# Kernel optimization log

Measured on AMD Instinct MI355X. Metric: run time of the kernel, lower is better.

Reference implementation:

```python
import jax, jax.numpy as jnp
import numpy as np

NUM_FIELDS = 26

def setup_inputs() -> dict:
    key = jax.random.key(0)
    ks = jax.random.split(key, 8)
    B, F, D, V, d, af = 4096, NUM_FIELDS, 13, 100000, 64, 64
    return {
        "sparse_feat": jax.random.randint(ks[0], (B, F), 0, V, dtype=jnp.int32),
        "dense_feat": jax.random.uniform(ks[1], (B, D), dtype=jnp.float32),
        "embed_table": jax.random.normal(ks[2], (V, d), dtype=jnp.float32) * 0.05,
        "lin_table": jax.random.normal(ks[3], (V,), dtype=jnp.float32) * 0.05,
        "w_dense": jax.random.normal(ks[4], (D,), dtype=jnp.float32) * 0.1,
        "bias": jnp.zeros((1,), dtype=jnp.float32),
        "W1": jax.random.normal(ks[5], (d, af), dtype=jnp.float32) * (1.0 / np.sqrt(d)),
        "b1": jnp.zeros((af,), dtype=jnp.float32),
        "w2": jax.random.normal(ks[6], (af,), dtype=jnp.float32) * (1.0 / np.sqrt(af)),
        "p": jax.random.normal(ks[7], (d,), dtype=jnp.float32) * (1.0 / np.sqrt(d)),
    }

def reference(sparse_feat, dense_feat, embed_table, lin_table, w_dense, bias, W1, b1, w2, p):
    # Embedding lookup: [B, F, d]
    emb = embed_table[sparse_feat]
    # Linear part: per-field scalar weights + dense linear + bias -> [B]
    linear_out = lin_table[sparse_feat].sum(axis=1) + dense_feat @ w_dense + bias[0]
    # Pairwise interactions i<j (static indices): [B, P, d]
    i_idx, j_idx = np.triu_indices(NUM_FIELDS, k=1)
    att_x = emb[:, i_idx, :] * emb[:, j_idx, :]
    # Attention MLP: Linear(d, af) + ReLU + Linear(af, 1, no bias) -> [B, P]
    h = jax.nn.relu(jnp.einsum('bpd,da->bpa', att_x, W1) + b1)
    att_w = jnp.einsum('bpa,a->bp', h, w2)
    att_score = jax.nn.softmax(att_w, axis=1)
    # Softmax-weighted sum over pairs -> [B, d], then final projection p -> [B]
    att_out = jnp.einsum('bpd,bp->bd', att_x, att_score)
    fm_att_out = att_out @ p
    return linear_out + fm_att_out
```

## Files before the change

### kernel.cpp

```cpp
#include <hip/hip_runtime.h>
#include <math.h>


#define NF 26
#define NP 325
#define NMT 21
#define ED 64
#define AF 64
#define NDENSE 13
#define WPB 4
#define BLOCK (WPB * 64)
#define ESTRIDE 72

typedef __attribute__((ext_vector_type(8))) _Float16 half8;
typedef __attribute__((ext_vector_type(4))) float f32x4;

__device__ __forceinline__ void wsync() {
    __builtin_amdgcn_fence(__ATOMIC_ACQ_REL, "workgroup");
    __builtin_amdgcn_wave_barrier();
}

__global__ void prep_kernel(const float* __restrict__ W1,
                            _Float16* __restrict__ w1t,
                            unsigned short* __restrict__ tab)
{
    int t = threadIdx.x;
    for (int idx = t; idx < ED * AF; idx += 256) {
        int d = idx >> 6, a = idx & 63;
        w1t[a * ED + d] = (_Float16)W1[idx];
    }
    if (t < NMT * 16) {
        unsigned short v = 0;
        if (t < NP) {
            int rem = t, i = 0;
            while (rem >= NF - 1 - i) { rem -= NF - 1 - i; ++i; }
            v = (unsigned short)(i | ((i + 1 + rem) << 8));
        }
        tab[t] = v;
    }
}

__global__ __launch_bounds__(BLOCK, 4)
void afm_kernel(const int*   __restrict__ sparse,
                const float* __restrict__ dense,
                const float* __restrict__ etab,
                const float* __restrict__ ltab,
                const float* __restrict__ wdense,
                const float* __restrict__ bias,
                const float* __restrict__ b1,
                const float* __restrict__ w2,
                const float* __restrict__ proj,
                const _Float16* __restrict__ w1t,
                const unsigned short* __restrict__ tab,
                float*       __restrict__ out,
                int B)
{
    const int t    = threadIdx.x;
    const int wave = t >> 6;
    const int lane = t & 63;
    const int qd   = lane >> 4;
    const int ln   = lane & 15;

    const int r = blockIdx.x * WPB + wave;
    if (r >= B) return;

    __shared__ alignas(16) _Float16 emb_all[WPB][NF][ESTRIDE];
    _Float16 (* __restrict__ emb)[ESTRIDE] = emb_all[wave];

    half8 bfr[4][2];
    #pragma unroll
    for (int nt = 0; nt < 4; ++nt)
        #pragma unroll
        for (int kh = 0; kh < 2; ++kh)
            bfr[nt][kh] = *(const half8*)(w1t + (nt * 16 + ln) * ED + kh * 32 + qd * 8);

    float4 b1v4[4], w2v4[4];
    #pragma unroll
    for (int nt = 0; nt < 4; ++nt) {
        b1v4[nt] = *(const float4*)(b1 + nt * 16 + qd * 4);
        w2v4[nt] = *(const float4*)(w2 + nt * 16 + qd * 4);
    }

    const int* __restrict__ srow = sparse + r * NF;
    for (int task = lane; task < NF * 8; task += 64) {
        int f = task >> 3, c = task & 7;
        const float* src = etab + (size_t)srow[f] * ED + c * 8;
        float4 v0 = *(const float4*)(src);
        float4 v1 = *(const float4*)(src + 4);
        half8 h = { (_Float16)v0.x, (_Float16)v0.y, (_Float16)v0.z, (_Float16)v0.w,
                    (_Float16)v1.x, (_Float16)v1.y, (_Float16)v1.z, (_Float16)v1.w };
        *(half8*)(&emb[f][c * 8]) = h;
    }

    float lin = 0.f;
    if (lane < NF) {
        lin = ltab[srow[lane]];
    } else if (lane >= 32 && lane < 32 + NDENSE) {
        int k = lane - 32;
        lin = dense[r * NDENSE + k] * wdense[k];
    }
    #pragma unroll
    for (int off = 32; off >= 1; off >>= 1) lin += __shfl_xor(lin, off, 64);
    lin += bias[0];

    wsync();

    float m = -INFINITY, l = 0.f;
    half8 acc0 = { (_Float16)0.f, (_Float16)0.f, (_Float16)0.f, (_Float16)0.f,
                   (_Float16)0.f, (_Float16)0.f, (_Float16)0.f, (_Float16)0.f };
    half8 acc1 = acc0;

    unsigned pp = tab[ln];
    int fi = pp & 0xff, fj = pp >> 8;
    half8 ei0 = *(const half8*)(&emb[fi][qd * 8]);
    half8 ei1 = *(const half8*)(&emb[fi][32 + qd * 8]);
    half8 ej0 = *(const half8*)(&emb[fj][qd * 8]);
    half8 ej1 = *(const half8*)(&emb[fj][32 + qd * 8]);

    for (int mt = 0; mt < NMT; ++mt) {
        half8 x0 = ei0 * ej0;
        half8 x1 = ei1 * ej1;

        if (mt + 1 < NMT) {
            unsigned np = tab[(mt + 1) * 16 + ln];
            int nfi = np & 0xff, nfj = np >> 8;
            ei0 = *(const half8*)(&emb[nfi][qd * 8]);
            ei1 = *(const half8*)(&emb[nfi][32 + qd * 8]);
            ej0 = *(const half8*)(&emb[nfj][qd * 8]);
            ej1 = *(const half8*)(&emb[nfj][32 + qd * 8]);
        }

        float lg = 0.f;
        #pragma unroll
        for (int nt = 0; nt < 4; ++nt) {
            f32x4 acc = { b1v4[nt].x, b1v4[nt].y, b1v4[nt].z, b1v4[nt].w };
            acc = __builtin_amdgcn_mfma_f32_16x16x32_f16(bfr[nt][0], x0, acc, 0, 0, 0);
            acc = __builtin_amdgcn_mfma_f32_16x16x32_f16(bfr[nt][1], x1, acc, 0, 0, 0);
            lg = fmaf(fmaxf(acc[0], 0.f), w2v4[nt].x, lg);
            lg = fmaf(fmaxf(acc[1], 0.f), w2v4[nt].y, lg);
            lg = fmaf(fmaxf(acc[2], 0.f), w2v4[nt].z, lg);
            lg = fmaf(fmaxf(acc[3], 0.f), w2v4[nt].w, lg);
        }
        lg += __shfl_xor(lg, 16, 64);
        lg += __shfl_xor(lg, 32, 64);

        const int p0 = mt * 16 + ln;
        if (p0 >= NP) lg = -INFINITY;

        float mn    = fmaxf(m, lg);
        float alpha = __expf(m - mn);
        float e     = __expf(lg - mn);
        l = l * alpha + e;
        m = mn;
        _Float16 ah = (_Float16)alpha, eh = (_Float16)e;
        half8 a8 = { ah, ah, ah, ah, ah, ah, ah, ah };
        half8 e8 = { eh, eh, eh, eh, eh, eh, eh, eh };
        acc0 = acc0 * a8 + x0 * e8;
        acc1 = acc1 * a8 + x1 * e8;
    }

    float mg = m;
    #pragma unroll
    for (int off = 1; off <= 8; off <<= 1) mg = fmaxf(mg, __shfl_xor(mg, off, 64));
    const float fac = __expf(m - mg);
    float lsum = l * fac;
    #pragma unroll
    for (int off = 1; off <= 8; off <<= 1) lsum += __shfl_xor(lsum, off, 64);

    float4 pa = *(const float4*)(proj + qd * 8);
    float4 pb = *(const float4*)(proj + qd * 8 + 4);
    float4 pc = *(const float4*)(proj + 32 + qd * 8);
    float4 pd = *(const float4*)(proj + 32 + qd * 8 + 4);
    float rr = (float)acc0[0] * pa.x + (float)acc0[1] * pa.y
             + (float)acc0[2] * pa.z + (float)acc0[3] * pa.w
             + (float)acc0[4] * pb.x + (float)acc0[5] * pb.y
             + (float)acc0[6] * pb.z + (float)acc0[7] * pb.w
             + (float)acc1[0] * pc.x + (float)acc1[1] * pc.y
             + (float)acc1[2] * pc.z + (float)acc1[3] * pc.w
             + (float)acc1[4] * pd.x + (float)acc1[5] * pd.y
             + (float)acc1[6] * pd.z + (float)acc1[7] * pd.w;
    rr *= fac;
    #pragma unroll
    for (int off = 1; off <= 32; off <<= 1) rr += __shfl_xor(rr, off, 64);

    if (lane == 0) out[r] = lin + rr / lsum;
}

extern "C" void kernel_launch(void* const* d_in, const int* in_sizes, int n_in,
                              void* d_out, int out_size, void* d_ws, size_t ws_size,
                              hipStream_t stream) {
    const int*   sparse = (const int*)  d_in[0];
    const float* dense  = (const float*)d_in[1];
    const float* etab   = (const float*)d_in[2];
    const float* ltab   = (const float*)d_in[3];
    const float* wdense = (const float*)d_in[4];
    const float* bias   = (const float*)d_in[5];
    const float* W1     = (const float*)d_in[6];
    const float* b1     = (const float*)d_in[7];
    const float* w2     = (const float*)d_in[8];
    const float* proj   = (const float*)d_in[9];
    float* outp = (float*)d_out;

    _Float16*       w1t = (_Float16*)d_ws;
    unsigned short* tab = (unsigned short*)((char*)d_ws + 8192);

    const int B = in_sizes[0] / NF;

    prep_kernel<<<dim3(1), dim3(256), 0, stream>>>(W1, w1t, tab);
    afm_kernel<<<dim3((B + WPB - 1) / WPB), dim3(BLOCK), 0, stream>>>(
        sparse, dense, etab, ltab, wdense, bias, b1, w2, proj, w1t, tab, outp, B);
    (void)n_in; (void)out_size; (void)ws_size;
}
```

Before: 116.0 us.

## Fold W1 transpose and pair table prep into main kernel via shared memory

Drops the separate single-block prep kernel. Each block now converts and transposes W1 to fp16 and builds the pair-index table in its own shared memory, behind a block-wide barrier. The per-tile logit reduction is also split into independent partial sums, which shortens the FMA dependency chain. This removes one kernel launch and the serial prep step ahead of the main kernel. In exchange, every block redoes the 4K-element W1 conversion and the table build, uses more LDS, and needs a __syncthreads where a wave-local sync was enough before.

New measurement: 113.0 us. 2.6% less time.

```diff
diff --git a/kernel.cpp b/kernel.cpp
--- a/kernel.cpp
+++ b/kernel.cpp
@@ -11,34 +11,10 @@
 #define WPB 4
 #define BLOCK (WPB * 64)
 #define ESTRIDE 72
+#define WSTRIDE 72
 
 typedef __attribute__((ext_vector_type(8))) _Float16 half8;
 typedef __attribute__((ext_vector_type(4))) float f32x4;
-
-__device__ __forceinline__ void wsync() {
-    __builtin_amdgcn_fence(__ATOMIC_ACQ_REL, "workgroup");
-    __builtin_amdgcn_wave_barrier();
-}
-
-__global__ void prep_kernel(const float* __restrict__ W1,
-                            _Float16* __restrict__ w1t,
-                            unsigned short* __restrict__ tab)
-{
-    int t = threadIdx.x;
-    for (int idx = t; idx < ED * AF; idx += 256) {
-        int d = idx >> 6, a = idx & 63;
-        w1t[a * ED + d] = (_Float16)W1[idx];
-    }
-    if (t < NMT * 16) {
-        unsigned short v = 0;
-        if (t < NP) {
-            int rem = t, i = 0;
-            while (rem >= NF - 1 - i) { rem -= NF - 1 - i; ++i; }
-            v = (unsigned short)(i | ((i + 1 + rem) << 8));
-        }
-        tab[t] = v;
-    }
-}
 
 __global__ __launch_bounds__(BLOCK, 4)
 void afm_kernel(const int*   __restrict__ sparse,
@@ -47,11 +23,10 @@
                 const float* __restrict__ ltab,
                 const float* __restrict__ wdense,
                 const float* __restrict__ bias,
+                const float* __restrict__ W1,
                 const float* __restrict__ b1,
                 const float* __restrict__ w2,
                 const float* __restrict__ proj,
-                const _Float16* __restrict__ w1t,
-                const unsigned short* __restrict__ tab,
                 float*       __restrict__ out,
                 int B)
 {
@@ -61,56 +36,76 @@
     const int qd   = lane >> 4;
     const int ln   = lane & 15;
 
+    __shared__ alignas(16) _Float16       w1t_s[AF][WSTRIDE];
+    __shared__              unsigned short tab_s[NMT * 16];
+    __shared__ alignas(16) _Float16       emb_all[WPB][NF][ESTRIDE];
+
+    for (int idx = t; idx < ED * AF; idx += BLOCK) {
+        int d = idx >> 6, a = idx & 63;
+        w1t_s[a][d] = (_Float16)W1[idx];
+    }
+    for (int p = t; p < NMT * 16; p += BLOCK) {
+        unsigned short v = 0;
+        if (p < NP) {
+            int rem = p, i = 0;
+            while (rem >= NF - 1 - i) { rem -= NF - 1 - i; ++i; }
+            v = (unsigned short)(i | ((i + 1 + rem) << 8));
+        }
+        tab_s[p] = v;
+    }
+
     const int r = blockIdx.x * WPB + wave;
-    if (r >= B) return;
-
-    __shared__ alignas(16) _Float16 emb_all[WPB][NF][ESTRIDE];
+    const bool active = (r < B);
+
     _Float16 (* __restrict__ emb)[ESTRIDE] = emb_all[wave];
+    float lin = 0.f;
+    float4 b1v4[4], w2v4[4];
+
+    if (active) {
+        const int* __restrict__ srow = sparse + r * NF;
+        for (int task = lane; task < NF * 8; task += 64) {
+            int f = task >> 3, c = task & 7;
+            const float* src = etab + (size_t)srow[f] * ED + c * 8;
+            float4 v0 = *(const float4*)(src);
+            float4 v1 = *(const float4*)(src + 4);
+            half8 h = { (_Float16)v0.x, (_Float16)v0.y, (_Float16)v0.z, (_Float16)v0.w,
+                        (_Float16)v1.x, (_Float16)v1.y, (_Float16)v1.z, (_Float16)v1.w };
+            *(half8*)(&emb[f][c * 8]) = h;
+        }
+
+        #pragma unroll
+        for (int nt = 0; nt < 4; ++nt) {
+            b1v4[nt] = *(const float4*)(b1 + nt * 16 + qd * 4);
+            w2v4[nt] = *(const float4*)(w2 + nt * 16 + qd * 4);
+        }
+
+        if (lane < NF) {
+            lin = ltab[srow[lane]];
+        } else if (lane >= 32 && lane < 32 + NDENSE) {
+            int k = lane - 32;
+            lin = dense[r * NDENSE + k] * wdense[k];
+        }
+        #pragma unroll
+        for (int off = 32; off >= 1; off >>= 1) lin += __shfl_xor(lin, off, 64);
+        lin += bias[0];
+    }
+
+    __syncthreads();
+    if (!active) return;
 
     half8 bfr[4][2];
     #pragma unroll
     for (int nt = 0; nt < 4; ++nt)
         #pragma unroll
         for (int kh = 0; kh < 2; ++kh)
-            bfr[nt][kh] = *(const half8*)(w1t + (nt * 16 + ln) * ED + kh * 32 + qd * 8);
-
-    float4 b1v4[4], w2v4[4];
-    #pragma unroll
-    for (int nt = 0; nt < 4; ++nt) {
-        b1v4[nt] = *(const float4*)(b1 + nt * 16 + qd * 4);
-        w2v4[nt] = *(const float4*)(w2 + nt * 16 + qd * 4);
-    }
-
-    const int* __restrict__ srow = sparse + r * NF;
-    for (int task = lane; task < NF * 8; task += 64) {
-        int f = task >> 3, c = task & 7;
-        const float* src = etab + (size_t)srow[f] * ED + c * 8;
-        float4 v0 = *(const float4*)(src);
-        float4 v1 = *(const float4*)(src + 4);
-        half8 h = { (_Float16)v0.x, (_Float16)v0.y, (_Float16)v0.z, (_Float16)v0.w,
-                    (_Float16)v1.x, (_Float16)v1.y, (_Float16)v1.z, (_Float16)v1.w };
-        *(half8*)(&emb[f][c * 8]) = h;
-    }
-
-    float lin = 0.f;
-    if (lane < NF) {
-        lin = ltab[srow[lane]];
-    } else if (lane >= 32 && lane < 32 + NDENSE) {
-        int k = lane - 32;
-        lin = dense[r * NDENSE + k] * wdense[k];
-    }
-    #pragma unroll
-    for (int off = 32; off >= 1; off >>= 1) lin += __shfl_xor(lin, off, 64);
-    lin += bias[0];
-
-    wsync();
+            bfr[nt][kh] = *(const half8*)(&w1t_s[nt * 16 + ln][kh * 32 + qd * 8]);
 
     float m = -INFINITY, l = 0.f;
     half8 acc0 = { (_Float16)0.f, (_Float16)0.f, (_Float16)0.f, (_Float16)0.f,
                    (_Float16)0.f, (_Float16)0.f, (_Float16)0.f, (_Float16)0.f };
     half8 acc1 = acc0;
 
-    unsigned pp = tab[ln];
+    unsigned pp = tab_s[ln];
     int fi = pp & 0xff, fj = pp >> 8;
     half8 ei0 = *(const half8*)(&emb[fi][qd * 8]);
     half8 ei1 = *(const half8*)(&emb[fi][32 + qd * 8]);
@@ -122,7 +117,7 @@
         half8 x1 = ei1 * ej1;
 
         if (mt + 1 < NMT) {
-            unsigned np = tab[(mt + 1) * 16 + ln];
+            unsigned np = tab_s[(mt + 1) * 16 + ln];
             int nfi = np & 0xff, nfj = np >> 8;
             ei0 = *(const half8*)(&emb[nfi][qd * 8]);
             ei1 = *(const half8*)(&emb[nfi][32 + qd * 8]);
@@ -130,17 +125,17 @@
             ej1 = *(const half8*)(&emb[nfj][32 + qd * 8]);
         }
 
-        float lg = 0.f;
+        float lgp[4];
         #pragma unroll
         for (int nt = 0; nt < 4; ++nt) {
             f32x4 acc = { b1v4[nt].x, b1v4[nt].y, b1v4[nt].z, b1v4[nt].w };
             acc = __builtin_amdgcn_mfma_f32_16x16x32_f16(bfr[nt][0], x0, acc, 0, 0, 0);
             acc = __builtin_amdgcn_mfma_f32_16x16x32_f16(bfr[nt][1], x1, acc, 0, 0, 0);
-            lg = fmaf(fmaxf(acc[0], 0.f), w2v4[nt].x, lg);
-            lg = fmaf(fmaxf(acc[1], 0.f), w2v4[nt].y, lg);
-            lg = fmaf(fmaxf(acc[2], 0.f), w2v4[nt].z, lg);
-            lg = fmaf(fmaxf(acc[3], 0.f), w2v4[nt].w, lg);
-        }
+            float u = fmaf(fmaxf(acc[1], 0.f), w2v4[nt].y, fmaxf(acc[0], 0.f) * w2v4[nt].x);
+            float v = fmaf(fmaxf(acc[3], 0.f), w2v4[nt].w, fmaxf(acc[2], 0.f) * w2v4[nt].z);
+            lgp[nt] = u + v;
+        }
+        float lg = (lgp[0] + lgp[1]) + (lgp[2] + lgp[3]);
         lg += __shfl_xor(lg, 16, 64);
         lg += __shfl_xor(lg, 32, 64);
 
@@ -201,13 +196,9 @@
     const float* proj   = (const float*)d_in[9];
     float* outp = (float*)d_out;
 
-    _Float16*       w1t = (_Float16*)d_ws;
-    unsigned short* tab = (unsigned short*)((char*)d_ws + 8192);
-
     const int B = in_sizes[0] / NF;
 
-    prep_kernel<<<dim3(1), dim3(256), 0, stream>>>(W1, w1t, tab);
     afm_kernel<<<dim3((B + WPB - 1) / WPB), dim3(BLOCK), 0, stream>>>(
-        sparse, dense, etab, ltab, wdense, bias, b1, w2, proj, w1t, tab, outp, B);
-    (void)n_in; (void)out_size; (void)ws_size;
+        sparse, dense, etab, ltab, wdense, bias, W1, b1, w2, proj, outp, B);
+    (void)n_in; (void)out_size; (void)d_ws; (void)ws_size;
 }
```
